# Optimization experiments

Hardware: AMD Instinct MI355X
Metric: run time of the kernel (lower is better)

Reference implementation:

```python
import jax, jax.numpy as jnp
import numpy as np

N = 768                       # atoms
E = N * (N - 1)               # complete directed graph edges
DIM = 64                      # hidden dim
CUT = 5.0                     # rbf high
NC = 50                       # n_centers = ceil(5/0.1)
ODIM = 1                      # output_dim
NCONV = 3
_centers_np = np.linspace(0.0, CUT, NC)
CENTERS = jnp.asarray(_centers_np, jnp.float32)
GAP = float(_centers_np[1] - _centers_np[0])
RO_IN = 2 * ODIM + NC         # readout input: 2*output_dim + rbf fan_out = 52


def softplus_bt(x, beta, thr):
    # torch.nn.Softplus(beta, threshold): linear above threshold
    bx = beta * x
    return jnp.where(bx > thr, x, jax.nn.softplus(bx) / beta)


def rbf(d):
    # exp(-(1/gap) * (d - mu_k)^2); d: (..., 1) -> (..., NC)
    return jnp.exp((-1.0 / GAP) * (d - CENTERS) ** 2)


def setup_inputs() -> dict:
    key = jax.random.key(0)
    ks = jax.random.split(key, 24)
    atom_types = jax.random.randint(ks[0], (N,), 0, 100)
    edge_distances = jax.random.uniform(ks[1], (E, 1), jnp.float32) * CUT
    # complete directed graph, edge order matches the nested i,j loop (i!=j)
    ii = np.repeat(np.arange(N), N)
    jj = np.tile(np.arange(N), N)
    m = ii != jj
    src = jnp.asarray(ii[m], jnp.int32)
    dst = jnp.asarray(jj[m], jnp.int32)

    def p(k, shape, fan):
        return jax.random.normal(k, shape, jnp.float32) / np.sqrt(fan)

    embedding = p(ks[2], (100, DIM), DIM).at[0].set(0.0)  # padding_idx=0
    L = NCONV
    return {
        'atom_types': atom_types, 'edge_distances': edge_distances,
        'src': src, 'dst': dst, 'embedding': embedding,
        'w1': p(ks[3], (L, DIM, DIM), DIM),                 # node_layer1 (no bias)
        'pw1': p(ks[4], (L, NC, DIM), NC), 'pb1': p(ks[5], (L, DIM), NC),
        'pw2': p(ks[6], (L, DIM, DIM), DIM), 'pb2': p(ks[7], (L, DIM), DIM),
        'qw1': p(ks[8], (L, DIM, DIM), DIM), 'qb1': p(ks[9], (L, DIM), DIM),
        'qw2': p(ks[10], (L, DIM, DIM), DIM), 'qb2': p(ks[11], (L, DIM), DIM),
        'au_w1': p(ks[12], (DIM, 64), DIM), 'au_b1': p(ks[13], (64,), DIM),
        'au_w2': p(ks[14], (64, ODIM), 64), 'au_b2': p(ks[15], (ODIM,), 64),
        'ro_w1': p(ks[16], (RO_IN, 64), RO_IN), 'ro_b1': p(ks[17], (64,), RO_IN),
        'ro_w2': p(ks[18], (64, 2), 64), 'ro_b2': p(ks[19], (2,), 64),
    }


def reference(atom_types, edge_distances, src, dst, embedding,
              w1, pw1, pb1, pw2, pb2, qw1, qb1, qw2, qb2,
              au_w1, au_b1, au_w2, au_b2, ro_w1, ro_b1, ro_w2, ro_b2):
    h = embedding[atom_types]                       # (N, DIM)
    rbf_out = rbf(edge_distances)                   # (E, NC)
    for l in range(NCONV):
        nw = h @ w1[l]                              # node weights (N, DIM)
        e = softplus_bt(rbf_out @ pw1[l] + pb1[l], 0.5, 14) @ pw2[l] + pb2[l]  # (E, DIM)
        msg = nw[src] * e                           # gather-mul (E, DIM)
        agg = jax.ops.segment_sum(msg, dst, num_segments=N)  # scatter-sum (N, DIM)
        upd = softplus_bt(agg @ qw1[l] + qb1[l], 0.5, 14) @ qw2[l] + qb2[l]
        h = h + upd
    # atom_update with ShiftSoftplus (beta=1, shift=2, threshold=20)
    ha = softplus_bt(h @ au_w1 + au_b1, 1.0, 20) - jnp.log(jnp.float32(2.0))
    ha = ha @ au_w2 + au_b2                         # (N, ODIM)
    # readout over all ordered pairs i!=j, in edge order == (src, dst)
    edge_feat = jnp.concatenate([ha[src], ha[dst], rbf_out], axis=-1)  # (E, 52)
    logits = jax.nn.relu(edge_feat @ ro_w1 + ro_b1) @ ro_w2 + ro_b2    # (E, 2)
    return jax.nn.softmax(logits, axis=-1)
```

## Files before the change

### kernel.cpp

```cpp
#include <hip/hip_runtime.h>
#include <hip/hip_fp16.h>

#define NATOMS 768
#define NM1    767
#define NEDGE  (768*767)
#define DIM    64
#define NC     50
#define GAPF   (5.0f/49.0f)
#define NIGAP  (-49.0f/5.0f)
#define G      512
#define STEPF  (5.0f/511.0f)
#define INVSTEP (511.0f/5.0f)
#define LN2F   0.693147180559945f

#define WS_H     0
#define WS_NWA   49152
#define WS_NWB   73728
#define WS_HA    98304
#define WS_DISTT 99328
#define WS_TT    689152

__device__ __forceinline__ float softplus05(float x) {
    float bx = 0.5f * x;
    return (bx > 14.0f) ? x : 2.0f * __logf(1.0f + __expf(bx));
}
__device__ __forceinline__ int lane_bcast_i(int v, int l) {
    return __builtin_amdgcn_readlane(v, l);
}
__device__ __forceinline__ float lane_bcast_f(float v, int l) {
    return __uint_as_float((unsigned)__builtin_amdgcn_readlane((int)__float_as_uint(v), l));
}

__global__ __launch_bounds__(256)
void k_pre(const int* __restrict__ types, const float* __restrict__ dist,
           const float* __restrict__ emb, const float* __restrict__ w1all,
           const float* __restrict__ pw1, const float* __restrict__ pb1,
           const float* __restrict__ pw2, const float* __restrict__ pb2,
           const float* __restrict__ row1, const float* __restrict__ rob1,
           float* __restrict__ ws) {
    __shared__ float s_t[4 * 64];
    __shared__ float s_tile[64][65];
    const int tid = threadIdx.x, widx = tid >> 6, c = tid & 63;
    float*  h     = ws + WS_H;
    __half* nwh   = (__half*)(ws + WS_NWA);
    float*  distT = ws + WS_DISTT;
    __half* TTh   = (__half*)(ws + WS_TT);
    const int b = blockIdx.x;

    if (b < 512) {
        const int w = b * 4 + widx, tbl = w >> 9, g = w & 511;
        const float d = g * STEPF;
        float val;
        if (tbl < 3) {
            const float* W1 = pw1 + tbl * NC * DIM;
            float t1 = pb1[tbl * DIM + c];
            for (int k = 0; k < NC; ++k) {
                float x = d - GAPF * (float)k;
                t1 = fmaf(__expf(NIGAP * x * x), W1[k * DIM + c], t1);
            }
            s_t[widx * 64 + c] = softplus05(t1);
            const float* W2 = pw2 + tbl * DIM * DIM;
            val = pb2[tbl * DIM + c];
            #pragma unroll 8
            for (int k = 0; k < DIM; ++k)
                val = fmaf(s_t[widx * 64 + k], W2[k * DIM + c], val);
        } else {
            val = rob1[c];
            for (int k = 0; k < NC; ++k) {
                float x = d - GAPF * (float)k;
                val = fmaf(__expf(NIGAP * x * x), row1[(2 + k) * DIM + c], val);
            }
        }
        __half* TTt = TTh + tbl * (G * DIM * 2);
        TTt[(g * DIM + c) * 2] = __float2half(val);
        if (g > 0) TTt[((g - 1) * DIM + c) * 2 + 1] = __float2half(val);
    } else if (b < 704) {
        const int i = (b - 512) * 4 + widx;
        float hv = emb[types[i] * DIM + c];
        h[i * DIM + c] = hv;
        s_t[widx * 64 + c] = hv;
        float acc = 0.0f;
        #pragma unroll 8
        for (int k = 0; k < DIM; ++k)
            acc = fmaf(s_t[widx * 64 + k], w1all[k * DIM + c], acc);
        nwh[i * DIM + c] = __float2half(acc);
    } else {
        const int t = b - 704;
        const int I0 = (t / 12) * 64, J0 = (t % 12) * 64;
        #pragma unroll 4
        for (int r = 0; r < 16; ++r) {
            const int i = I0 + widx * 16 + r;
            const int j = J0 + c;
            s_tile[widx * 16 + r][c] =
                (i == j) ? 0.0f : dist[i * NM1 + (j - (j > i))];
        }
        __syncthreads();
        #pragma unroll 4
        for (int r = 0; r < 16; ++r) {
            const int j = J0 + widx * 16 + r;
            const int i = I0 + c;
            distT[j * NATOMS + i] = s_tile[c][widx * 16 + r];
        }
    }
}

__global__ __launch_bounds__(512)
void k_edgeupd(const __half2* __restrict__ TTl, const float* __restrict__ distT,
               const __half* __restrict__ nwin,
               const float* __restrict__ qw1, const float* __restrict__ qb1,
               const float* __restrict__ qw2, const float* __restrict__ qb2,
               float* __restrict__ h,
               const float* __restrict__ wnext, __half* __restrict__ nwout,
               const float* __restrict__ auw1, const float* __restrict__ aub1,
               const float* __restrict__ auw2, const float* __restrict__ aub2,
               float* __restrict__ ha, int last) {
    __shared__ float s_part[8][64];
    __shared__ float s_upd[192];
    const int tid = threadIdx.x, widx = tid >> 6, c = tid & 63;
    const int j = blockIdx.x;
    const int s0 = widx * 96;

    const char* TTb = (const char*)TTl + c * 4;
    float csum = 0.0f;
    {
        float d = distT[j * NATOMS + s0 + c];
        float pos = d * INVSTEP;
        int g = (int)pos;
        g = (g < 0) ? 0 : ((g > 510) ? 510 : g);
        float f = pos - (float)g;
        int kx = g * 256;
        #pragma unroll 8
        for (int it = 0; it < 64; ++it) {
            int kxu = lane_bcast_i(kx, it);
            float fu = lane_bcast_f(f, it);
            float2 tt = __half22float2(*(const __half2*)(TTb + kxu));
            float e = fmaf(fu, tt.y - tt.x, tt.x);
            float nwv = __half2float(nwin[(s0 + it) * DIM + c]);
            csum = fmaf(e, nwv, csum);
        }
    }
    {
        float d = distT[j * NATOMS + s0 + 64 + (c & 31)];
        float pos = d * INVSTEP;
        int g = (int)pos;
        g = (g < 0) ? 0 : ((g > 510) ? 510 : g);
        float f = pos - (float)g;
        int kx = g * 256;
        #pragma unroll 8
        for (int it = 0; it < 32; ++it) {
            int kxu = lane_bcast_i(kx, it);
            float fu = lane_bcast_f(f, it);
            float2 tt = __half22float2(*(const __half2*)(TTb + kxu));
            float e = fmaf(fu, tt.y - tt.x, tt.x);
            float nwv = __half2float(nwin[(s0 + 64 + it) * DIM + c]);
            csum = fmaf(e, nwv, csum);
        }
    }
    s_part[widx][c] = csum;
    __syncthreads();

    if (widx == 0) {
        float tot = 0.0f;
        #pragma unroll
        for (int w8 = 0; w8 < 8; ++w8) tot += s_part[w8][c];
        float2 t0 = __half22float2(*(const __half2*)TTb);
        tot -= t0.x * __half2float(nwin[j * DIM + c]);
        s_upd[c] = tot;
        float t = qb1[c];
        #pragma unroll 8
        for (int k = 0; k < DIM; ++k) t = fmaf(s_upd[k], qw1[k * DIM + c], t);
        s_upd[64 + c] = softplus05(t);
        float o = qb2[c];
        #pragma unroll 8
        for (int k = 0; k < DIM; ++k) o = fmaf(s_upd[64 + k], qw2[k * DIM + c], o);
        float hn = h[j * DIM + c] + o;
        h[j * DIM + c] = hn;
        s_upd[128 + c] = hn;
        if (!last) {
            float v = 0.0f;
            #pragma unroll 8
            for (int k = 0; k < DIM; ++k) v = fmaf(s_upd[128 + k], wnext[k * DIM + c], v);
            nwout[j * DIM + c] = __float2half(v);
        } else {
            float t2 = aub1[c];
            #pragma unroll 8
            for (int k = 0; k < DIM; ++k) t2 = fmaf(s_upd[128 + k], auw1[k * DIM + c], t2);
            t2 = ((t2 > 20.0f) ? t2 : __logf(1.0f + __expf(t2))) - LN2F;
            float v = t2 * auw2[c];
            #pragma unroll
            for (int s = 32; s > 0; s >>= 1) v += __shfl_down(v, s, 64);
            if (c == 0) ha[j] = v + aub2[0];
        }
    }
}

__global__ __launch_bounds__(256)
void k_ro(const float* __restrict__ dist, const int* __restrict__ src,
          const int* __restrict__ dst, const float* __restrict__ ha,
          const __half2* __restrict__ TTro,
          const float* __restrict__ row1, const float* __restrict__ row2,
          const float* __restrict__ rob2, float* __restrict__ out) {
    __shared__ float4 s_pre[4][64];
    __shared__ float s_h[4][16 * 65];
    __shared__ float s_w2[128];
    const int tid = threadIdx.x, widx = tid >> 6, c = tid & 63;
    if (tid < 128) s_w2[tid] = row2[tid];
    __syncthreads();
    const int ebase = (blockIdx.x * 4 + widx) * 64;
    {
        int eg = ebase + c;
        float d = dist[eg];
        float pos = d * INVSTEP;
        int kk = (int)pos;
        kk = (kk < 0) ? 0 : ((kk > 510) ? 510 : kk);
        float fa = ha[src[eg]], fb = ha[dst[eg]];
        s_pre[widx][c] = make_float4(__int_as_float(kk * 256), pos - (float)kk, fa, fb);
    }
    const char* TTb2 = (const char*)TTro + c * 4;
    const float wa = row1[c], wb = row1[DIM + c];
    const int e2 = (c >> 1) & 15, p2 = c & 1, kh = c >> 5;
    const float bias2 = (kh == 0) ? rob2[p2] : 0.0f;
    float* sh = s_h[widx];
    #pragma unroll
    for (int ch = 0; ch < 4; ++ch) {
        #pragma unroll 4
        for (int e = 0; e < 16; ++e) {
            float4 p = s_pre[widx][ch * 16 + e];
            float2 tt = __half22float2(*(const __half2*)(TTb2 + __float_as_int(p.x)));
            float hv = fmaf(p.y, tt.y - tt.x, tt.x);
            hv = fmaf(p.z, wa, hv);
            hv = fmaf(p.w, wb, hv);
            sh[e * 65 + c] = fmaxf(hv, 0.0f);
        }
        float lsum = bias2;
        #pragma unroll 8
        for (int k8 = 0; k8 < 32; ++k8) {
            int k = kh * 32 + k8;
            lsum = fmaf(sh[e2 * 65 + k], s_w2[2 * k + p2], lsum);
        }
        lsum += __shfl_xor(lsum, 32, 64);
        float other = __shfl_xor(lsum, 1, 64);
        float m = fmaxf(lsum, other);
        float ea = __expf(lsum - m), eb = __expf(other - m);
        float r = ea / (ea + eb);
        if (c < 32) out[ebase * 2 + ch * 32 + c] = r;
    }
}

extern "C" void kernel_launch(void* const* d_in, const int* in_sizes, int n_in,
                              void* d_out, int out_size, void* d_ws, size_t ws_size,
                              hipStream_t stream) {
    const int*   types = (const int*)d_in[0];
    const float* dist  = (const float*)d_in[1];
    const int*   srcI  = (const int*)d_in[2];
    const int*   dstI  = (const int*)d_in[3];
    const float* emb   = (const float*)d_in[4];
    const float* w1    = (const float*)d_in[5];
    const float* pw1   = (const float*)d_in[6];
    const float* pb1   = (const float*)d_in[7];
    const float* pw2   = (const float*)d_in[8];
    const float* pb2   = (const float*)d_in[9];
    const float* qw1   = (const float*)d_in[10];
    const float* qb1   = (const float*)d_in[11];
    const float* qw2   = (const float*)d_in[12];
    const float* qb2   = (const float*)d_in[13];
    const float* auw1  = (const float*)d_in[14];
    const float* aub1  = (const float*)d_in[15];
    const float* auw2  = (const float*)d_in[16];
    const float* aub2  = (const float*)d_in[17];
    const float* row1  = (const float*)d_in[18];
    const float* rob1  = (const float*)d_in[19];
    const float* row2  = (const float*)d_in[20];
    const float* rob2  = (const float*)d_in[21];

    float* ws   = (float*)d_ws;
    float* outp = (float*)d_out;
    const __half2* TT = (const __half2*)(ws + WS_TT);
    __half* nwbuf[2] = { (__half*)(ws + WS_NWA), (__half*)(ws + WS_NWB) };

    k_pre<<<848, 256, 0, stream>>>(types, dist, emb, w1, pw1, pb1, pw2, pb2,
                                   row1, rob1, ws);
    for (int l = 0; l < 3; ++l) {
        k_edgeupd<<<768, 512, 0, stream>>>(TT + l * (G * DIM),
            ws + WS_DISTT, nwbuf[l & 1],
            qw1 + l * DIM * DIM, qb1 + l * DIM,
            qw2 + l * DIM * DIM, qb2 + l * DIM,
            ws + WS_H,
            (l < 2) ? (w1 + (l + 1) * DIM * DIM) : w1, nwbuf[(l + 1) & 1],
            auw1, aub1, auw2, aub2, ws + WS_HA, (l == 2) ? 1 : 0);
    }
    k_ro<<<2301, 256, 0, stream>>>(dist, srcI, dstI, ws + WS_HA, TT + 3 * (G * DIM),
                                   row1, row2, rob2, outp);
}
```

Measured before the change: 190.7 us.

## Interleave node-weight rows as half2 pairs and broadcast readout params via lanes

```diff
diff --git a/kernel.cpp b/kernel.cpp
--- a/kernel.cpp
+++ b/kernel.cpp
@@ -83,7 +83,7 @@
         #pragma unroll 8
         for (int k = 0; k < DIM; ++k)
             acc = fmaf(s_t[widx * 64 + k], w1all[k * DIM + c], acc);
-        nwh[i * DIM + c] = __float2half(acc);
+        nwh[(i >> 1) * 128 + c * 2 + (i & 1)] = __float2half(acc);
     } else {
         const int t = b - 704;
         const int I0 = (t / 12) * 64, J0 = (t % 12) * 64;
@@ -106,7 +106,7 @@
 
 __global__ __launch_bounds__(512)
 void k_edgeupd(const __half2* __restrict__ TTl, const float* __restrict__ distT,
-               const __half* __restrict__ nwin,
+               const __half2* __restrict__ nwin,
                const float* __restrict__ qw1, const float* __restrict__ qb1,
                const float* __restrict__ qw2, const float* __restrict__ qb2,
                float* __restrict__ h,
@@ -129,14 +129,20 @@
         g = (g < 0) ? 0 : ((g > 510) ? 510 : g);
         float f = pos - (float)g;
         int kx = g * 256;
-        #pragma unroll 8
-        for (int it = 0; it < 64; ++it) {
-            int kxu = lane_bcast_i(kx, it);
-            float fu = lane_bcast_f(f, it);
-            float2 tt = __half22float2(*(const __half2*)(TTb + kxu));
-            float e = fmaf(fu, tt.y - tt.x, tt.x);
-            float nwv = __half2float(nwin[(s0 + it) * DIM + c]);
-            csum = fmaf(e, nwv, csum);
+        const __half2* nwrow = nwin + (s0 >> 1) * 64 + c;
+        #pragma unroll 8
+        for (int t = 0; t < 32; ++t) {
+            int kx0 = lane_bcast_i(kx, 2 * t);
+            int kx1 = lane_bcast_i(kx, 2 * t + 1);
+            float f0 = lane_bcast_f(f, 2 * t);
+            float f1 = lane_bcast_f(f, 2 * t + 1);
+            float2 ta = __half22float2(*(const __half2*)(TTb + kx0));
+            float2 tb = __half22float2(*(const __half2*)(TTb + kx1));
+            float2 nwf = __half22float2(nwrow[t * 64]);
+            float e0 = fmaf(f0, ta.y - ta.x, ta.x);
+            float e1 = fmaf(f1, tb.y - tb.x, tb.x);
+            csum = fmaf(e0, nwf.x, csum);
+            csum = fmaf(e1, nwf.y, csum);
         }
     }
     {
@@ -146,14 +152,20 @@
         g = (g < 0) ? 0 : ((g > 510) ? 510 : g);
         float f = pos - (float)g;
         int kx = g * 256;
-        #pragma unroll 8
-        for (int it = 0; it < 32; ++it) {
-            int kxu = lane_bcast_i(kx, it);
-            float fu = lane_bcast_f(f, it);
-            float2 tt = __half22float2(*(const __half2*)(TTb + kxu));
-            float e = fmaf(fu, tt.y - tt.x, tt.x);
-            float nwv = __half2float(nwin[(s0 + 64 + it) * DIM + c]);
-            csum = fmaf(e, nwv, csum);
+        const __half2* nwrow = nwin + ((s0 + 64) >> 1) * 64 + c;
+        #pragma unroll 8
+        for (int t = 0; t < 16; ++t) {
+            int kx0 = lane_bcast_i(kx, 2 * t);
+            int kx1 = lane_bcast_i(kx, 2 * t + 1);
+            float f0 = lane_bcast_f(f, 2 * t);
+            float f1 = lane_bcast_f(f, 2 * t + 1);
+            float2 ta = __half22float2(*(const __half2*)(TTb + kx0));
+            float2 tb = __half22float2(*(const __half2*)(TTb + kx1));
+            float2 nwf = __half22float2(nwrow[t * 64]);
+            float e0 = fmaf(f0, ta.y - ta.x, ta.x);
+            float e1 = fmaf(f1, tb.y - tb.x, tb.x);
+            csum = fmaf(e0, nwf.x, csum);
+            csum = fmaf(e1, nwf.y, csum);
         }
     }
     s_part[widx][c] = csum;
@@ -164,7 +176,8 @@
         #pragma unroll
         for (int w8 = 0; w8 < 8; ++w8) tot += s_part[w8][c];
         float2 t0 = __half22float2(*(const __half2*)TTb);
-        tot -= t0.x * __half2float(nwin[j * DIM + c]);
+        float nwj = __half2float(((const __half*)nwin)[(j >> 1) * 128 + c * 2 + (j & 1)]);
+        tot -= t0.x * nwj;
         s_upd[c] = tot;
         float t = qb1[c];
         #pragma unroll 8
@@ -180,7 +193,7 @@
             float v = 0.0f;
             #pragma unroll 8
             for (int k = 0; k < DIM; ++k) v = fmaf(s_upd[128 + k], wnext[k * DIM + c], v);
-            nwout[j * DIM + c] = __float2half(v);
+            nwout[(j >> 1) * 128 + c * 2 + (j & 1)] = __float2half(v);
         } else {
             float t2 = aub1[c];
             #pragma unroll 8
@@ -200,21 +213,24 @@
           const __half2* __restrict__ TTro,
           const float* __restrict__ row1, const float* __restrict__ row2,
           const float* __restrict__ rob2, float* __restrict__ out) {
-    __shared__ float4 s_pre[4][64];
     __shared__ float s_h[4][16 * 65];
     __shared__ float s_w2[128];
     const int tid = threadIdx.x, widx = tid >> 6, c = tid & 63;
     if (tid < 128) s_w2[tid] = row2[tid];
     __syncthreads();
     const int ebase = (blockIdx.x * 4 + widx) * 64;
+
+    int kxv; float ff, fa, fb;
     {
         int eg = ebase + c;
         float d = dist[eg];
         float pos = d * INVSTEP;
         int kk = (int)pos;
         kk = (kk < 0) ? 0 : ((kk > 510) ? 510 : kk);
-        float fa = ha[src[eg]], fb = ha[dst[eg]];
-        s_pre[widx][c] = make_float4(__int_as_float(kk * 256), pos - (float)kk, fa, fb);
+        kxv = kk * 256;
+        ff = pos - (float)kk;
+        fa = ha[src[eg]];
+        fb = ha[dst[eg]];
     }
     const char* TTb2 = (const char*)TTro + c * 4;
     const float wa = row1[c], wb = row1[DIM + c];
@@ -223,13 +239,17 @@
     float* sh = s_h[widx];
     #pragma unroll
     for (int ch = 0; ch < 4; ++ch) {
-        #pragma unroll 4
+        #pragma unroll 8
         for (int e = 0; e < 16; ++e) {
-            float4 p = s_pre[widx][ch * 16 + e];
-            float2 tt = __half22float2(*(const __half2*)(TTb2 + __float_as_int(p.x)));
-            float hv = fmaf(p.y, tt.y - tt.x, tt.x);
-            hv = fmaf(p.z, wa, hv);
-            hv = fmaf(p.w, wb, hv);
+            const int le = ch * 16 + e;
+            int kxu   = lane_bcast_i(kxv, le);
+            float fu  = lane_bcast_f(ff, le);
+            float fau = lane_bcast_f(fa, le);
+            float fbu = lane_bcast_f(fb, le);
+            float2 tt = __half22float2(*(const __half2*)(TTb2 + kxu));
+            float hv = fmaf(fu, tt.y - tt.x, tt.x);
+            hv = fmaf(fau, wa, hv);
+            hv = fmaf(fbu, wb, hv);
             sh[e * 65 + c] = fmaxf(hv, 0.0f);
         }
         float lsum = bias2;
@@ -276,7 +296,7 @@
     float* ws   = (float*)d_ws;
     float* outp = (float*)d_out;
     const __half2* TT = (const __half2*)(ws + WS_TT);
-    __half* nwbuf[2] = { (__half*)(ws + WS_NWA), (__half*)(ws + WS_NWB) };
+    __half2* nwbuf[2] = { (__half2*)(ws + WS_NWA), (__half2*)(ws + WS_NWB) };
 
     k_pre<<<848, 256, 0, stream>>>(types, dist, emb, w1, pw1, pb1, pw2, pb2,
                                    row1, rob1, ws);
@@ -286,7 +306,7 @@
             qw1 + l * DIM * DIM, qb1 + l * DIM,
             qw2 + l * DIM * DIM, qb2 + l * DIM,
             ws + WS_H,
-            (l < 2) ? (w1 + (l + 1) * DIM * DIM) : w1, nwbuf[(l + 1) & 1],
+            (l < 2) ? (w1 + (l + 1) * DIM * DIM) : w1, (__half*)nwbuf[(l + 1) & 1],
             auw1, aub1, auw2, aub2, ws + WS_HA, (l == 2) ? 1 : 0);
     }
     k_ro<<<2301, 256, 0, stream>>>(dist, srcI, dstI, ws + WS_HA, TT + 3 * (G * DIM),
```

Result: faster. 185.5 us (-2.7%).
